# Optimization experiments

Hardware: AMD Instinct MI355X
Metric: run time of the kernel (lower is better)

## Reference

```python
import jax, jax.numpy as jnp
import numpy as np

H = 4       # hidden size
IN = 906    # input size
B = 128
T = 512


def _lstm_dir(xp, W_hh):
    """Run a single-direction LSTM. xp: [B, T, 4H] precomputed input projection
    (x @ W_ih^T + b_ih + b_hh). Returns hidden states [B, T, H].
    Torch gate order: i, f, g, o."""
    Bb = xp.shape[0]
    h0 = jnp.zeros((Bb, H), xp.dtype)
    c0 = jnp.zeros((Bb, H), xp.dtype)

    def step(carry, g_t):
        h, c = carry
        g = g_t + h @ W_hh.T                      # [B, 4H]
        i, f, gg, o = jnp.split(g, 4, axis=-1)
        i = jax.nn.sigmoid(i)
        f = jax.nn.sigmoid(f)
        gg = jnp.tanh(gg)
        o = jax.nn.sigmoid(o)
        c = f * c + i * gg
        h = o * jnp.tanh(c)
        return (h, c), h

    xs = jnp.swapaxes(xp, 0, 1)                   # [T, B, 4H]
    _, hs = jax.lax.scan(step, (h0, c0), xs)      # hs: [T, B, H]
    return jnp.swapaxes(hs, 0, 1)                 # [B, T, H]


def setup_inputs() -> dict:
    key = jax.random.key(0)
    ks = jax.random.split(key, 12)
    s = 1.0 / np.sqrt(H)  # torch nn.LSTM init scale
    d = {
        "x": jax.random.normal(ks[0], (B, T, IN), jnp.float32),
        "W_ih_f": jax.random.normal(ks[1], (4 * H, IN), jnp.float32) * s,
        "W_hh_f": jax.random.normal(ks[2], (4 * H, H), jnp.float32) * s,
        "b_ih_f": jax.random.normal(ks[3], (4 * H,), jnp.float32) * s,
        "b_hh_f": jax.random.normal(ks[4], (4 * H,), jnp.float32) * s,
        "W_ih_b": jax.random.normal(ks[5], (4 * H, IN), jnp.float32) * s,
        "W_hh_b": jax.random.normal(ks[6], (4 * H, H), jnp.float32) * s,
        "b_ih_b": jax.random.normal(ks[7], (4 * H,), jnp.float32) * s,
        "b_hh_b": jax.random.normal(ks[8], (4 * H,), jnp.float32) * s,
        "W_out": jax.random.normal(ks[9], (2, 2 * H), jnp.float32) * s,
        "b_out": jax.random.normal(ks[10], (2,), jnp.float32) * s,
    }
    return d


def reference(x, W_ih_f, W_hh_f, b_ih_f, b_hh_f, W_ih_b, W_hh_b, b_ih_b, b_hh_b, W_out, b_out):
    # forward direction
    xp_f = x @ W_ih_f.T + (b_ih_f + b_hh_f)       # [B, T, 4H]
    out_f = _lstm_dir(xp_f, W_hh_f)               # [B, T, H]
    # backward direction: process reversed sequence, then flip back to align time
    xr = x[:, ::-1]
    xp_b = xr @ W_ih_b.T + (b_ih_b + b_hh_b)
    out_b = _lstm_dir(xp_b, W_hh_b)[:, ::-1]      # [B, T, H]
    # r_out[:, -1, :] = concat(fwd last step, bwd output at last time index)
    last = jnp.concatenate([out_f[:, -1], out_b[:, -1]], axis=-1)  # [B, 2H]
    return last @ W_out.T + b_out                 # [B, 2]
```

## Files before the change

kernel.cpp:

```cpp
#include <hip/hip_runtime.h>

#define IN 906
#define TT 512
#define NB 128

__device__ __forceinline__ float fsigm(float x) {
    float e = __builtin_amdgcn_exp2f(-1.4426950408889634f * x);
    return __builtin_amdgcn_rcpf(1.f + e);
}
__device__ __forceinline__ float ftanh(float x) {
    float e = __builtin_amdgcn_exp2f(-2.8853900817779268f * x);
    return 2.f * __builtin_amdgcn_rcpf(1.f + e) - 1.f;
}
template <int M>
__device__ __forceinline__ float quad_bcast(float v) {
    constexpr int ctrl = M | (M << 2) | (M << 4) | (M << 6);
    return __int_as_float(
        __builtin_amdgcn_mov_dpp(__float_as_int(v), ctrl, 0xf, 0xf, true));
}

__global__ __launch_bounds__(256, 2)
void gemm_xp(const float* __restrict__ x, const float* __restrict__ W,
             const float* __restrict__ b1, const float* __restrict__ b2,
             float* __restrict__ xp)
{
    const int tid = threadIdx.x;
    const int l   = tid & 63;
    const size_t row0 = (size_t)blockIdx.x * 32 + (size_t)(tid >> 6) * 8;

    float acc[128];
#pragma unroll
    for (int i = 0; i < 128; ++i) acc[i] = 0.f;

    const int kl = l * 2;

#pragma unroll
    for (int s = 0; s < 8; ++s) {
        const int k = s * 128 + kl;
        float2 wv[16];
        float2 xv[8];
        if (s < 7) {
#pragma unroll
            for (int jj = 0; jj < 16; ++jj)
                wv[jj] = *(const float2*)(W + jj * IN + k);
#pragma unroll
            for (int r = 0; r < 8; ++r)
                xv[r] = *(const float2*)(x + (row0 + r) * IN + k);
        } else {
            const int  kc = (k < IN) ? k : 904;
            const bool ok = (k < IN);
#pragma unroll
            for (int jj = 0; jj < 16; ++jj) {
                float2 t = *(const float2*)(W + jj * IN + kc);
                wv[jj].x = ok ? t.x : 0.f;
                wv[jj].y = ok ? t.y : 0.f;
            }
#pragma unroll
            for (int r = 0; r < 8; ++r)
                xv[r] = *(const float2*)(x + (row0 + r) * IN + kc);
        }
#pragma unroll
        for (int r = 0; r < 8; ++r)
#pragma unroll
            for (int jj = 0; jj < 16; ++jj) {
                acc[r * 16 + jj] = fmaf(xv[r].x, wv[jj].x, acc[r * 16 + jj]);
                acc[r * 16 + jj] = fmaf(xv[r].y, wv[jj].y, acc[r * 16 + jj]);
            }
    }

    float v1[64];
#pragma unroll
    for (int i = 0; i < 64; ++i) {
        float lo = acc[2 * i], hi = acc[2 * i + 1];
        float mi = (l & 1) ? hi : lo;
        float ot = (l & 1) ? lo : hi;
        v1[i] = mi + __shfl_xor(ot, 1);
    }
    float v2[32];
#pragma unroll
    for (int i = 0; i < 32; ++i) {
        float lo = v1[2 * i], hi = v1[2 * i + 1];
        float mi = (l & 2) ? hi : lo;
        float ot = (l & 2) ? lo : hi;
        v2[i] = mi + __shfl_xor(ot, 2);
    }
    float v3[16];
#pragma unroll
    for (int i = 0; i < 16; ++i) {
        float lo = v2[2 * i], hi = v2[2 * i + 1];
        float mi = (l & 4) ? hi : lo;
        float ot = (l & 4) ? lo : hi;
        v3[i] = mi + __shfl_xor(ot, 4);
    }
    float v4[8];
#pragma unroll
    for (int i = 0; i < 8; ++i) {
        float lo = v3[2 * i], hi = v3[2 * i + 1];
        float mi = (l & 8) ? hi : lo;
        float ot = (l & 8) ? lo : hi;
        v4[i] = mi + __shfl_xor(ot, 8);
    }
    float v5[4];
#pragma unroll
    for (int i = 0; i < 4; ++i) {
        float lo = v4[2 * i], hi = v4[2 * i + 1];
        float mi = (l & 16) ? hi : lo;
        float ot = (l & 16) ? lo : hi;
        v5[i] = mi + __shfl_xor(ot, 16);
    }
    float v6[2];
#pragma unroll
    for (int i = 0; i < 2; ++i) {
        float lo = v5[2 * i], hi = v5[2 * i + 1];
        float mi = (l & 32) ? hi : lo;
        float ot = (l & 32) ? lo : hi;
        v6[i] = mi + __shfl_xor(ot, 32);
    }

    const int jo = l & 15;
    const int g  = (l >> 4) & 3;
    const int pj = (jo & 3) * 4 + (jo >> 2);
    const float bias = b1[jo] + b2[jo];
#pragma unroll
    for (int p = 0; p < 2; ++p)
        xp[(row0 + (size_t)(p * 4 + g)) * 16 + pj] = v6[p] + bias;
}

__global__ __launch_bounds__(256)
void frec(const float* __restrict__ xp, const float* __restrict__ x,
          const float* __restrict__ Whh, const float* __restrict__ Wb,
          const float* __restrict__ bb1, const float* __restrict__ bb2,
          const float* __restrict__ Wout, const float* __restrict__ bout,
          float* __restrict__ out)
{
    __shared__ float bg[16][12];
    const int tid = threadIdx.x;

    float h0 = 0.f, h1 = 0.f, h2 = 0.f, h3 = 0.f;

    if (tid >= 64) {
        const int gl = tid - 64;
        const int r  = gl >> 4;
        const int bq = gl & 15;
        const int b  = blockIdx.x * 16 + bq;
        const int gr = (r < 4) ? r : r + 4;
        const float2* __restrict__ xr  = (const float2*)(x + ((size_t)b * TT + (TT - 1)) * IN);
        const float2* __restrict__ wrp = (const float2*)(Wb + gr * IN);
        float s0 = 0.f, s1 = 0.f;
        int j = 0;
        for (; j + 8 <= 453; j += 8) {
#pragma unroll
            for (int u = 0; u < 8; ++u) {
                float2 a = xr[j + u];
                float2 w = wrp[j + u];
                s0 = fmaf(a.x, w.x, s0);
                s1 = fmaf(a.y, w.y, s1);
            }
        }
        for (; j < 453; ++j) {
            float2 a = xr[j];
            float2 w = wrp[j];
            s0 = fmaf(a.x, w.x, s0);
            s1 = fmaf(a.y, w.y, s1);
        }
        bg[bq][r] = s0 + s1 + bb1[gr] + bb2[gr];
    } else {
        const int k = tid & 3;
        const int b = blockIdx.x * 16 + (tid >> 2);

        float Wi[4], Wf4[4], Wg[4], Wo[4];
#pragma unroll
        for (int m = 0; m < 4; ++m) {
            Wi[m]  = Whh[(k)      * 4 + m];
            Wf4[m] = Whh[(4 + k)  * 4 + m];
            Wg[m]  = Whh[(8 + k)  * 4 + m];
            Wo[m]  = Whh[(12 + k) * 4 + m];
        }

        const float4* __restrict__ xq = (const float4*)xp;
        const size_t base = (size_t)b * TT * 4 + k;

        float4 pf[16];
#pragma unroll
        for (int i = 0; i < 16; ++i) pf[i] = xq[base + (size_t)i * 4];

        float c = 0.f;
        for (int t = 0; t < TT; t += 16) {
#pragma unroll
            for (int u = 0; u < 16; ++u) {
                float4 cur = pf[u];
                int tn = t + 16 + u;
                int tc = (tn < TT) ? tn : (TT - 1);
                pf[u] = xq[base + (size_t)tc * 4];

                float gi = cur.x + h0 * Wi[0]  + h1 * Wi[1]  + h2 * Wi[2]  + h3 * Wi[3];
                float gf = cur.y + h0 * Wf4[0] + h1 * Wf4[1] + h2 * Wf4[2] + h3 * Wf4[3];
                float gg = cur.z + h0 * Wg[0]  + h1 * Wg[1]  + h2 * Wg[2]  + h3 * Wg[3];
                float go = cur.w + h0 * Wo[0]  + h1 * Wo[1]  + h2 * Wo[2]  + h3 * Wo[3];

                float si = fsigm(gi);
                float sf = fsigm(gf);
                float tg = ftanh(gg);
                float so = fsigm(go);

                c = sf * c + si * tg;
                float h = so * ftanh(c);

                h0 = quad_bcast<0>(h);
                h1 = quad_bcast<1>(h);
                h2 = quad_bcast<2>(h);
                h3 = quad_bcast<3>(h);
            }
        }
    }

    __syncthreads();

    if (tid < 64) {
        const int k  = tid & 3;
        const int bq = tid >> 2;
        const int b  = blockIdx.x * 16 + bq;

        float gib = bg[bq][k];
        float ggb = bg[bq][4 + k];
        float gob = bg[bq][8 + k];
        float hbk = fsigm(gob) * ftanh(fsigm(gib) * ftanh(ggb));
        float hb0 = quad_bcast<0>(hbk);
        float hb1 = quad_bcast<1>(hbk);
        float hb2 = quad_bcast<2>(hbk);
        float hb3 = quad_bcast<3>(hbk);

        float o0 = bout[0]
                 + h0  * Wout[0]  + h1  * Wout[1]  + h2  * Wout[2]  + h3  * Wout[3]
                 + hb0 * Wout[4]  + hb1 * Wout[5]  + hb2 * Wout[6]  + hb3 * Wout[7];
        float o1 = bout[1]
                 + h0  * Wout[8]  + h1  * Wout[9]  + h2  * Wout[10] + h3  * Wout[11]
                 + hb0 * Wout[12] + hb1 * Wout[13] + hb2 * Wout[14] + hb3 * Wout[15];

        if (k == 0) {
            out[b * 2 + 0] = o0;
            out[b * 2 + 1] = o1;
        }
    }
}

extern "C" void kernel_launch(void* const* d_in, const int* in_sizes, int n_in,
                              void* d_out, int out_size, void* d_ws, size_t ws_size,
                              hipStream_t stream)
{
    const float* x    = (const float*)d_in[0];
    const float* Wihf = (const float*)d_in[1];
    const float* Whhf = (const float*)d_in[2];
    const float* bihf = (const float*)d_in[3];
    const float* bhhf = (const float*)d_in[4];
    const float* Wihb = (const float*)d_in[5];
    const float* bihb = (const float*)d_in[7];
    const float* bhhb = (const float*)d_in[8];
    const float* Wout = (const float*)d_in[9];
    const float* bout = (const float*)d_in[10];

    float* xp = (float*)d_ws;

    gemm_xp<<<2048, 256, 0, stream>>>(x, Wihf, bihf, bhhf, xp);
    frec<<<8, 256, 0, stream>>>(xp, x, Whhf, Wihb, bihb, bhhb, Wout, bout,
                                (float*)d_out);
}
```

Before: 456.0 us.

## Halve rows per wave in input-projection GEMM and double-buffer slice loads

Each wave now handles 4 rows instead of 8, which halves the accumulator array and doubles the grid size. Launch bounds are raised to 3 blocks per SM so more waves can hide memory latency. The K loop now uses explicit double buffering, loading slice s+1 while the current slice is multiplied and accumulated. The trade-off is that W is re-read by twice as many waves, and the extra buffer adds register pressure.

```diff
diff --git a/kernel.cpp b/kernel.cpp
--- a/kernel.cpp
+++ b/kernel.cpp
@@ -19,36 +19,36 @@
         __builtin_amdgcn_mov_dpp(__float_as_int(v), ctrl, 0xf, 0xf, true));
 }
 
-__global__ __launch_bounds__(256, 2)
+__global__ __launch_bounds__(256, 3)
 void gemm_xp(const float* __restrict__ x, const float* __restrict__ W,
              const float* __restrict__ b1, const float* __restrict__ b2,
              float* __restrict__ xp)
 {
     const int tid = threadIdx.x;
     const int l   = tid & 63;
-    const size_t row0 = (size_t)blockIdx.x * 32 + (size_t)(tid >> 6) * 8;
-
-    float acc[128];
-#pragma unroll
-    for (int i = 0; i < 128; ++i) acc[i] = 0.f;
+    const size_t row0 = (size_t)blockIdx.x * 16 + (size_t)(tid >> 6) * 4;
+
+    float acc[64];
+#pragma unroll
+    for (int i = 0; i < 64; ++i) acc[i] = 0.f;
 
     const int kl = l * 2;
 
-#pragma unroll
-    for (int s = 0; s < 8; ++s) {
+    float2 wA[16], wB[16];
+    float2 xA[4],  xB[4];
+
+    auto load_slice = [&](int s, float2 (&wv)[16], float2 (&xv)[4]) {
         const int k = s * 128 + kl;
-        float2 wv[16];
-        float2 xv[8];
         if (s < 7) {
 #pragma unroll
             for (int jj = 0; jj < 16; ++jj)
                 wv[jj] = *(const float2*)(W + jj * IN + k);
 #pragma unroll
-            for (int r = 0; r < 8; ++r)
+            for (int r = 0; r < 4; ++r)
                 xv[r] = *(const float2*)(x + (row0 + r) * IN + k);
         } else {
-            const int  kc = (k < IN) ? k : 904;
             const bool ok = (k < IN);
+            const int  kc = ok ? k : 0;
 #pragma unroll
             for (int jj = 0; jj < 16; ++jj) {
                 float2 t = *(const float2*)(W + jj * IN + kc);
@@ -56,74 +56,83 @@
                 wv[jj].y = ok ? t.y : 0.f;
             }
 #pragma unroll
-            for (int r = 0; r < 8; ++r)
+            for (int r = 0; r < 4; ++r)
                 xv[r] = *(const float2*)(x + (row0 + r) * IN + kc);
         }
-#pragma unroll
-        for (int r = 0; r < 8; ++r)
+    };
+    auto mac_slice = [&](float2 (&wv)[16], float2 (&xv)[4]) {
+#pragma unroll
+        for (int r = 0; r < 4; ++r)
 #pragma unroll
             for (int jj = 0; jj < 16; ++jj) {
                 acc[r * 16 + jj] = fmaf(xv[r].x, wv[jj].x, acc[r * 16 + jj]);
                 acc[r * 16 + jj] = fmaf(xv[r].y, wv[jj].y, acc[r * 16 + jj]);
             }
-    }
-
-    float v1[64];
-#pragma unroll
-    for (int i = 0; i < 64; ++i) {
+    };
+
+    load_slice(0, wA, xA);
+#pragma unroll
+    for (int s = 0; s < 8; ++s) {
+        if (s + 1 < 8) {
+            if (s & 1) load_slice(s + 1, wA, xA);
+            else       load_slice(s + 1, wB, xB);
+        }
+        if (s & 1) mac_slice(wB, xB);
+        else       mac_slice(wA, xA);
+    }
+
+    float u1[32];
+#pragma unroll
+    for (int i = 0; i < 32; ++i) {
         float lo = acc[2 * i], hi = acc[2 * i + 1];
         float mi = (l & 1) ? hi : lo;
         float ot = (l & 1) ? lo : hi;
-        v1[i] = mi + __shfl_xor(ot, 1);
-    }
-    float v2[32];
-#pragma unroll
-    for (int i = 0; i < 32; ++i) {
-        float lo = v1[2 * i], hi = v1[2 * i + 1];
+        u1[i] = mi + __shfl_xor(ot, 1);
+    }
+    float u2[16];
+#pragma unroll
+    for (int i = 0; i < 16; ++i) {
+        float lo = u1[2 * i], hi = u1[2 * i + 1];
         float mi = (l & 2) ? hi : lo;
         float ot = (l & 2) ? lo : hi;
-        v2[i] = mi + __shfl_xor(ot, 2);
-    }
-    float v3[16];
-#pragma unroll
-    for (int i = 0; i < 16; ++i) {
-        float lo = v2[2 * i], hi = v2[2 * i + 1];
+        u2[i] = mi + __shfl_xor(ot, 2);
+    }
+    float u3[8];
+#pragma unroll
+    for (int i = 0; i < 8; ++i) {
+        float lo = u2[2 * i], hi = u2[2 * i + 1];
         float mi = (l & 4) ? hi : lo;
         float ot = (l & 4) ? lo : hi;
-        v3[i] = mi + __shfl_xor(ot, 4);
-    }
-    float v4[8];
-#pragma unroll
-    for (int i = 0; i < 8; ++i) {
-        float lo = v3[2 * i], hi = v3[2 * i + 1];
+        u3[i] = mi + __shfl_xor(ot, 4);
+    }
+    float u4[4];
+#pragma unroll
+    for (int i = 0; i < 4; ++i) {
+        float lo = u3[2 * i], hi = u3[2 * i + 1];
         float mi = (l & 8) ? hi : lo;
         float ot = (l & 8) ? lo : hi;
-        v4[i] = mi + __shfl_xor(ot, 8);
-    }
-    float v5[4];
-#pragma unroll
-    for (int i = 0; i < 4; ++i) {
-        float lo = v4[2 * i], hi = v4[2 * i + 1];
+        u4[i] = mi + __shfl_xor(ot, 8);
+    }
+    float u5[2];
+#pragma unroll
+    for (int i = 0; i < 2; ++i) {
+        float lo = u4[2 * i], hi = u4[2 * i + 1];
         float mi = (l & 16) ? hi : lo;
         float ot = (l & 16) ? lo : hi;
-        v5[i] = mi + __shfl_xor(ot, 16);
-    }
-    float v6[2];
-#pragma unroll
-    for (int i = 0; i < 2; ++i) {
-        float lo = v5[2 * i], hi = v5[2 * i + 1];
+        u5[i] = mi + __shfl_xor(ot, 16);
+    }
+    float tot;
+    {
+        float lo = u5[0], hi = u5[1];
         float mi = (l & 32) ? hi : lo;
         float ot = (l & 32) ? lo : hi;
-        v6[i] = mi + __shfl_xor(ot, 32);
+        tot = mi + __shfl_xor(ot, 32);
     }
 
     const int jo = l & 15;
     const int g  = (l >> 4) & 3;
     const int pj = (jo & 3) * 4 + (jo >> 2);
-    const float bias = b1[jo] + b2[jo];
-#pragma unroll
-    for (int p = 0; p < 2; ++p)
-        xp[(row0 + (size_t)(p * 4 + g)) * 16 + pj] = v6[p] + bias;
+    xp[(row0 + (size_t)g) * 16 + pj] = tot + b1[jo] + b2[jo];
 }
 
 __global__ __launch_bounds__(256)
@@ -261,7 +270,7 @@
 
     float* xp = (float*)d_ws;
 
-    gemm_xp<<<2048, 256, 0, stream>>>(x, Wihf, bihf, bhhf, xp);
+    gemm_xp<<<4096, 256, 0, stream>>>(x, Wihf, bihf, bhhf, xp);
     frec<<<8, 256, 0, stream>>>(xp, x, Whhf, Wihb, bihb, bhhb, Wout, bout,
                                 (float*)d_out);
 }
```

Measured after the change: 482.7 us. +5.9%, slower.
